# Kernel optimization log

Measured on AMD Instinct MI355X. Metric: run time of the kernel, lower is better.

Reference implementation:

```python
import jax, jax.numpy as jnp
import numpy as np

N_NODES = 50000
N_EDGES = 800000
IN_FEATS = 64
HIDDEN = 64
NUM_CLASSES = 32


def _graph_conv(x, src, dst, W, b, n_nodes):
    # DGL GraphConv, norm='both', allow_zero_in_degree=True:
    # out = D_in^{-1/2} * (A^T @ (D_out^{-1/2} * x)) @ W + b, degrees clamped to >=1
    e = src.shape[0]
    ones = jnp.ones((e,), dtype=x.dtype)
    out_deg = jax.ops.segment_sum(ones, src, num_segments=n_nodes)
    in_deg = jax.ops.segment_sum(ones, dst, num_segments=n_nodes)
    norm_src = jax.lax.rsqrt(jnp.maximum(out_deg, 1.0))[:, None]
    norm_dst = jax.lax.rsqrt(jnp.maximum(in_deg, 1.0))[:, None]
    h = x * norm_src                                   # [N, d]
    agg = jax.ops.segment_sum(h[src], dst, num_segments=n_nodes)  # gather+scatter over edges
    return (agg * norm_dst) @ W + b


def setup_inputs() -> dict:
    key = jax.random.key(0)
    k1, k2, k3, k4, k5 = jax.random.split(key, 5)
    features = jax.random.normal(k1, (N_NODES, IN_FEATS), dtype=jnp.float32)
    src = jax.random.randint(k2, (N_EDGES,), 0, N_NODES, dtype=jnp.int32)
    dst = jax.random.randint(k3, (N_EDGES,), 0, N_NODES, dtype=jnp.int32)
    W1 = jax.random.normal(k4, (IN_FEATS, HIDDEN), dtype=jnp.float32) * (1.0 / np.sqrt(IN_FEATS))
    b1 = jnp.zeros((HIDDEN,), dtype=jnp.float32)
    W2 = jax.random.normal(k5, (HIDDEN, NUM_CLASSES), dtype=jnp.float32) * (1.0 / np.sqrt(HIDDEN))
    b2 = jnp.zeros((NUM_CLASSES,), dtype=jnp.float32)
    return {"features": features, "src": src, "dst": dst,
            "W1": W1, "b1": b1, "W2": W2, "b2": b2}


def reference(features, src, dst, W1, b1, W2, b2) -> jnp.ndarray:
    n = features.shape[0]
    h = jax.nn.relu(_graph_conv(features, src, dst, W1, b1, n))
    out = _graph_conv(h, src, dst, W2, b2, n)
    # single canonical etype -> mean over one-element stack is identity
    return out
```

## Files before the change

### kernel.cpp

```cpp
#include <hip/hip_runtime.h>
#include <hip/hip_bf16.h>

#define N_NODES 50000
#define N_EDGES 800000
#define F 64
#define C 32
#define CAP 48

#define NPB   200
#define EPB   4000
#define NBUCK 196

#define G1_BLOCKS 2048

static __device__ __forceinline__ float bflo(int u) {
    return __uint_as_float(((unsigned)u) << 16);
}
static __device__ __forceinline__ float bfhi(int u) {
    return __uint_as_float(((unsigned)u) & 0xffff0000u);
}
static __device__ __forceinline__ unsigned short f2bf(float f) {
    __hip_bfloat16 h = __float2bfloat16(f);
    return *reinterpret_cast<unsigned short*>(&h);
}

__global__ void part_count_kernel(const int* __restrict__ src, const int* __restrict__ dst,
                                  int* __restrict__ bcnt_d, int* __restrict__ bcnt_s) {
    __shared__ int hd[NBUCK], hs[NBUCK];
    int t = threadIdx.x;
    for (int i = t; i < NBUCK; i += 256) { hd[i] = 0; hs[i] = 0; }
    __syncthreads();
    int b0 = blockIdx.x * EPB;
    for (int i = b0 + t; i < b0 + EPB; i += 256) {
        atomicAdd(&hd[dst[i] >> 8], 1);
        atomicAdd(&hs[src[i] >> 8], 1);
    }
    __syncthreads();
    for (int i = t; i < NBUCK; i += 256) {
        bcnt_d[i * NPB + blockIdx.x] = hd[i];
        bcnt_s[i * NPB + blockIdx.x] = hs[i];
    }
}

__global__ void part_scan_kernel(const int* __restrict__ bcnt_d, const int* __restrict__ bcnt_s,
                                 int* __restrict__ eoff_d, int* __restrict__ eoff_s,
                                 int* __restrict__ base_d, int* __restrict__ base_s) {
    __shared__ int tot_d[NBUCK], tot_s[NBUCK], bd[NBUCK + 1], bs[NBUCK + 1];
    int t = threadIdx.x;
    if (t < NBUCK) {
        int run = 0;
        for (int q = 0; q < NPB / 4; q++) {
            int4 v = *reinterpret_cast<const int4*>(bcnt_d + t * NPB + 4 * q);
            int4 o;
            o.x = run; run += v.x;
            o.y = run; run += v.y;
            o.z = run; run += v.z;
            o.w = run; run += v.w;
            *reinterpret_cast<int4*>(eoff_d + t * NPB + 4 * q) = o;
        }
        tot_d[t] = run;
        run = 0;
        for (int q = 0; q < NPB / 4; q++) {
            int4 v = *reinterpret_cast<const int4*>(bcnt_s + t * NPB + 4 * q);
            int4 o;
            o.x = run; run += v.x;
            o.y = run; run += v.y;
            o.z = run; run += v.z;
            o.w = run; run += v.w;
            *reinterpret_cast<int4*>(eoff_s + t * NPB + 4 * q) = o;
        }
        tot_s[t] = run;
    }
    __syncthreads();
    if (t == 0) {
        int r = 0;
        for (int b = 0; b < NBUCK; b++) { bd[b] = r; r += tot_d[b]; }
        bd[NBUCK] = r;
        r = 0;
        for (int b = 0; b < NBUCK; b++) { bs[b] = r; r += tot_s[b]; }
        bs[NBUCK] = r;
    }
    __syncthreads();
    if (t < NBUCK + 1) { base_d[t] = bd[t]; base_s[t] = bs[t]; }
}

__global__ void part_scatter_kernel(const int* __restrict__ src, const int* __restrict__ dst,
                                    const int* __restrict__ eoff_d, const int* __restrict__ eoff_s,
                                    const int* __restrict__ base_d, const int* __restrict__ base_s,
                                    int* __restrict__ edge_d, unsigned char* __restrict__ edge_s) {
    __shared__ int cd[NBUCK], cs[NBUCK];
    int t = threadIdx.x;
    for (int i = t; i < NBUCK; i += 256) {
        cd[i] = base_d[i] + eoff_d[i * NPB + blockIdx.x];
        cs[i] = base_s[i] + eoff_s[i * NPB + blockIdx.x];
    }
    __syncthreads();
    int b0 = blockIdx.x * EPB;
    for (int i = b0 + t; i < b0 + EPB; i += 256) {
        int d = dst[i], s = src[i];
        int p = atomicAdd(&cd[d >> 8], 1);
        edge_d[p] = ((d & 255) << 16) | s;
        int q = atomicAdd(&cs[s >> 8], 1);
        edge_s[q] = (unsigned char)(s & 255);
    }
}

__global__ void bucket_build_kernel(const int* __restrict__ edge_d,
                                    const unsigned char* __restrict__ edge_s,
                                    const int* __restrict__ base_d, const int* __restrict__ base_s,
                                    int* __restrict__ csr, int* __restrict__ cnt,
                                    float* __restrict__ norm_dst, float* __restrict__ norm_src) {
    __shared__ int cur[256];
    __shared__ int hs[256];
    int t = threadIdx.x;
    int bucket = blockIdx.x;
    cur[t] = 0;
    hs[t] = 0;
    __syncthreads();
    int lo = base_d[bucket], hi = base_d[bucket + 1];
    for (int i = lo + t; i < hi; i += 256) {
        int pd = edge_d[i];
        int dlow = pd >> 16;
        int s = pd & 0xFFFF;
        int pos = atomicAdd(&cur[dlow], 1);
        if (pos < CAP) csr[(size_t)(bucket * 256 + dlow) * CAP + pos] = s;
    }
    int slo = base_s[bucket], shi = base_s[bucket + 1];
    for (int i = slo + t; i < shi; i += 256) {
        atomicAdd(&hs[edge_s[i]], 1);
    }
    __syncthreads();
    int node = bucket * 256 + t;
    if (node < N_NODES) {
        int c = cur[t] < CAP ? cur[t] : CAP;
        cnt[node] = c;
        norm_dst[node] = rsqrtf(fmaxf((float)c, 1.0f));
        norm_src[node] = rsqrtf(fmaxf((float)hs[t], 1.0f));
    }
}

__global__ void gemm_y_kernel(const float* __restrict__ x,
                              const float* __restrict__ ns,
                              const float* __restrict__ W,
                              __hip_bfloat16* __restrict__ y) {
    __shared__ float sW[F * F];
    __shared__ float srow[16][F];
    int t = threadIdx.x;
    for (int i = t; i < F * F; i += 256) sW[i] = W[i];
    int j = t & 63;
    int w = t >> 6;
    int base = blockIdx.x * 16;
    for (int r = w; r < 16; r += 4) srow[r][j] = x[(size_t)(base + r) * F + j];
    __syncthreads();
    float a0 = 0, a1 = 0, a2 = 0, a3 = 0;
#pragma unroll
    for (int k = 0; k < F; k++) {
        float wv = sW[k * F + j];
        a0 += srow[w * 4 + 0][k] * wv;
        a1 += srow[w * 4 + 1][k] * wv;
        a2 += srow[w * 4 + 2][k] * wv;
        a3 += srow[w * 4 + 3][k] * wv;
    }
    int n0 = base + w * 4;
    y[(size_t)(n0 + 0) * F + j] = __float2bfloat16(a0 * ns[n0 + 0]);
    y[(size_t)(n0 + 1) * F + j] = __float2bfloat16(a1 * ns[n0 + 1]);
    y[(size_t)(n0 + 2) * F + j] = __float2bfloat16(a2 * ns[n0 + 2]);
    y[(size_t)(n0 + 3) * F + j] = __float2bfloat16(a3 * ns[n0 + 3]);
}

__global__ void gather64_gemv_kernel(const __hip_bfloat16* __restrict__ y,
                                     const int* __restrict__ csr,
                                     const int* __restrict__ cnt,
                                     const float* __restrict__ norm_dst,
                                     const float* __restrict__ norm_src,
                                     const float* __restrict__ b1,
                                     const float* __restrict__ W2,
                                     __hip_bfloat16* __restrict__ gt) {
    __shared__ float sW[F * C];
    int t = threadIdx.x;
    for (int i = t; i < F * C; i += 256) sW[i] = W2[i];
    __syncthreads();
    int w    = t >> 6;
    int lane = t & 63;
    int g  = lane >> 3;
    int fo = (lane & 7) * 8;
    int j    = lane & 31;
    int half = lane >> 5;
    const float4 b1a = *reinterpret_cast<const float4*>(b1 + fo);
    const float4 b1b = *reinterpret_cast<const float4*>(b1 + fo + 4);
    const unsigned short* ytab = reinterpret_cast<const unsigned short*>(y);

    for (int node = blockIdx.x * 4 + w; node < N_NODES; node += G1_BLOCKS * 4) {
        int n = cnt[node];
        const int* row = csr + (size_t)node * CAP;
        float a0 = 0.f, a1 = 0.f, a2 = 0.f, a3 = 0.f,
              a4 = 0.f, a5 = 0.f, a6 = 0.f, a7 = 0.f;

#define G1_ROUND(i)                                                          \
        {                                                                    \
            int ee = (i) * 8 + g;                                            \
            int rv = row[ee];                 \
            int ss = (ee < n) ? rv : 0;                                      \
            float m = (ee < n) ? 1.f : 0.f;                                  \
            const int4 v = *reinterpret_cast<const int4*>(                   \
                ytab + (size_t)ss * F + fo);                                 \
            a0 = fmaf(m, bflo(v.x), a0); a1 = fmaf(m, bfhi(v.x), a1);        \
            a2 = fmaf(m, bflo(v.y), a2); a3 = fmaf(m, bfhi(v.y), a3);        \
            a4 = fmaf(m, bflo(v.z), a4); a5 = fmaf(m, bfhi(v.z), a5);        \
            a6 = fmaf(m, bflo(v.w), a6); a7 = fmaf(m, bfhi(v.w), a7);        \
        }
        G1_ROUND(0)
        G1_ROUND(1)
        if (n > 16) {
            G1_ROUND(2)
            G1_ROUND(3)
            if (n > 32) {
                G1_ROUND(4)
                G1_ROUND(5)
            }
        }
#undef G1_ROUND

#define G1_RED(mk)                                                           \
        a0 += __shfl_xor(a0, mk); a1 += __shfl_xor(a1, mk);                  \
        a2 += __shfl_xor(a2, mk); a3 += __shfl_xor(a3, mk);                  \
        a4 += __shfl_xor(a4, mk); a5 += __shfl_xor(a5, mk);                  \
        a6 += __shfl_xor(a6, mk); a7 += __shfl_xor(a7, mk);
        G1_RED(8)
        G1_RED(16)
        G1_RED(32)
#undef G1_RED

        float nd = norm_dst[node], ns = norm_src[node];
        float hh[8];
        hh[0] = fmaxf(fmaf(a0, nd, b1a.x), 0.f) * ns;
        hh[1] = fmaxf(fmaf(a1, nd, b1a.y), 0.f) * ns;
        hh[2] = fmaxf(fmaf(a2, nd, b1a.z), 0.f) * ns;
        hh[3] = fmaxf(fmaf(a3, nd, b1a.w), 0.f) * ns;
        hh[4] = fmaxf(fmaf(a4, nd, b1b.x), 0.f) * ns;
        hh[5] = fmaxf(fmaf(a5, nd, b1b.y), 0.f) * ns;
        hh[6] = fmaxf(fmaf(a6, nd, b1b.z), 0.f) * ns;
        hh[7] = fmaxf(fmaf(a7, nd, b1b.w), 0.f) * ns;

        float o = 0.f;
#pragma unroll
        for (int k = 0; k < 32; k++) {
            float hv = __shfl(hh[k & 7], (half << 2) + (k >> 3));
            o = fmaf(hv, sW[(half * 32 + k) * C + j], o);
        }
        o += __shfl_down(o, 32);
        if (half == 0)
            __builtin_nontemporal_store(f2bf(o),
                reinterpret_cast<unsigned short*>(gt) + (size_t)node * C + j);
    }
}

__global__ void gather_out_kernel(const __hip_bfloat16* __restrict__ gt,
                                  const int* __restrict__ csr,
                                  const int* __restrict__ cnt,
                                  const float* __restrict__ norm_dst,
                                  const float* __restrict__ b2,
                                  float* __restrict__ out) {
    int t = threadIdx.x;
    int w = t >> 6;
    int lane = t & 63;
    int node = blockIdx.x * 4 + w;
    int g  = lane >> 3;
    int fo = (lane & 7) * 4;
    const unsigned short* tab = reinterpret_cast<const unsigned short*>(gt);
    int n = cnt[node];
    const int* row = csr + (size_t)node * CAP;
    float a0 = 0.f, a1 = 0.f, a2 = 0.f, a3 = 0.f;

#define G2_ROUND(i)                                                          \
    {                                                                        \
        int ee = (i) * 8 + g;                                                \
        int rv = row[ee];                                                    \
        int ss = (ee < n) ? rv : 0;                                          \
        float m = (ee < n) ? 1.f : 0.f;                                      \
        const int2 v = *reinterpret_cast<const int2*>(                       \
            tab + (size_t)ss * C + fo);                                      \
        a0 = fmaf(m, bflo(v.x), a0); a1 = fmaf(m, bfhi(v.x), a1);            \
        a2 = fmaf(m, bflo(v.y), a2); a3 = fmaf(m, bfhi(v.y), a3);            \
    }
    G2_ROUND(0)
    G2_ROUND(1)
    if (n > 16) {
        G2_ROUND(2)
        G2_ROUND(3)
        if (n > 32) {
            G2_ROUND(4)
            G2_ROUND(5)
        }
    }
#undef G2_ROUND

    a0 += __shfl_xor(a0, 8);  a1 += __shfl_xor(a1, 8);
    a2 += __shfl_xor(a2, 8);  a3 += __shfl_xor(a3, 8);
    a0 += __shfl_xor(a0, 16); a1 += __shfl_xor(a1, 16);
    a2 += __shfl_xor(a2, 16); a3 += __shfl_xor(a3, 16);
    a0 += __shfl_xor(a0, 32); a1 += __shfl_xor(a1, 32);
    a2 += __shfl_xor(a2, 32); a3 += __shfl_xor(a3, 32);

    if (lane < 8) {
        float nd = norm_dst[node];
        const float4 bb = *reinterpret_cast<const float4*>(b2 + fo);
        float o0 = fmaf(a0, nd, bb.x);
        float o1 = fmaf(a1, nd, bb.y);
        float o2 = fmaf(a2, nd, bb.z);
        float o3 = fmaf(a3, nd, bb.w);
        unsigned long long p0 = ((unsigned long long)__float_as_uint(o0)) |
                                ((unsigned long long)__float_as_uint(o1) << 32);
        unsigned long long p1 = ((unsigned long long)__float_as_uint(o2)) |
                                ((unsigned long long)__float_as_uint(o3) << 32);
        unsigned long long* po = reinterpret_cast<unsigned long long*>(
            out + (size_t)node * C + fo);
        __builtin_nontemporal_store(p0, po);
        __builtin_nontemporal_store(p1, po + 1);
    }
}

extern "C" void kernel_launch(void* const* d_in, const int* in_sizes, int n_in,
                              void* d_out, int out_size, void* d_ws, size_t ws_size,
                              hipStream_t stream) {
    const float* features = (const float*)d_in[0];
    const int*   src      = (const int*)d_in[1];
    const int*   dst      = (const int*)d_in[2];
    const float* W1       = (const float*)d_in[3];
    const float* b1       = (const float*)d_in[4];
    const float* W2       = (const float*)d_in[5];
    const float* b2       = (const float*)d_in[6];
    float* out = (float*)d_out;

    char* p = (char*)d_ws;
    float* norm_src = (float*)p;  p += (size_t)N_NODES * 4;
    float* norm_dst = (float*)p;  p += (size_t)N_NODES * 4;
    int*   cnt      = (int*)p;    p += (size_t)N_NODES * 4;
    int*   csr      = (int*)p;    p += (size_t)N_NODES * CAP * 4;
    __hip_bfloat16* y  = (__hip_bfloat16*)p;  p += (size_t)N_NODES * F * 2;
    __hip_bfloat16* gt = (__hip_bfloat16*)p;

    int* edge_d = (int*)y;
    unsigned char* edge_s = (unsigned char*)(edge_d + N_EDGES);
    int* q = (int*)gt;
    int* bcnt_d = q;                 q += NPB * NBUCK;
    int* bcnt_s = q;                 q += NPB * NBUCK;
    int* eoff_d = q;                 q += NPB * NBUCK;
    int* eoff_s = q;                 q += NPB * NBUCK;
    int* base_d = q;                 q += NBUCK + 1;
    int* base_s = q;

    part_count_kernel<<<NPB, 256, 0, stream>>>(src, dst, bcnt_d, bcnt_s);
    part_scan_kernel<<<1, 256, 0, stream>>>(bcnt_d, bcnt_s, eoff_d, eoff_s, base_d, base_s);
    part_scatter_kernel<<<NPB, 256, 0, stream>>>(src, dst, eoff_d, eoff_s, base_d, base_s,
                                                 edge_d, edge_s);
    bucket_build_kernel<<<NBUCK, 256, 0, stream>>>(edge_d, edge_s, base_d, base_s,
                                                   csr, cnt, norm_dst, norm_src);

    gemm_y_kernel<<<N_NODES / 16, 256, 0, stream>>>(features, norm_src, W1, y);
    gather64_gemv_kernel<<<G1_BLOCKS, 256, 0, stream>>>(y, csr, cnt, norm_dst,
                                                        norm_src, b1, W2, gt);

    gather_out_kernel<<<N_NODES / 4, 256, 0, stream>>>(gt, csr, cnt, norm_dst,
                                                       b2, out);
}
```

Baseline: 209.5 us.

## Software-pipeline CSR row loads and issue all gathers unconditionally in both gather kernels

Both gather kernels now prefetch the next node's count, norms and six CSR index slots while the current node's gathers are in flight. All six gather rounds are issued without branching, with masked-out lanes reading row 0. The output gather becomes a persistent grid-stride kernel with 2048 blocks instead of one block per four nodes. This is meant to hide index-load latency and raise memory-level parallelism, at the cost of extra loads for low-degree nodes and more registers.

After: 210.0 us. Within noise of the previous version (+0.2%).

```diff
diff --git a/kernel.cpp b/kernel.cpp
--- a/kernel.cpp
+++ b/kernel.cpp
@@ -11,7 +11,8 @@
 #define EPB   4000
 #define NBUCK 196
 
-#define G1_BLOCKS 2048
+#define G1_BLOCKS   2048
+#define GOUT_BLOCKS 2048
 
 static __device__ __forceinline__ float bflo(int u) {
     return __uint_as_float(((unsigned)u) << 16);
@@ -189,37 +190,61 @@
     const float4 b1a = *reinterpret_cast<const float4*>(b1 + fo);
     const float4 b1b = *reinterpret_cast<const float4*>(b1 + fo + 4);
     const unsigned short* ytab = reinterpret_cast<const unsigned short*>(y);
-
-    for (int node = blockIdx.x * 4 + w; node < N_NODES; node += G1_BLOCKS * 4) {
-        int n = cnt[node];
-        const int* row = csr + (size_t)node * CAP;
-        float a0 = 0.f, a1 = 0.f, a2 = 0.f, a3 = 0.f,
-              a4 = 0.f, a5 = 0.f, a6 = 0.f, a7 = 0.f;
-
-#define G1_ROUND(i)                                                          \
-        {                                                                    \
-            int ee = (i) * 8 + g;                                            \
-            int rv = row[ee];                 \
-            int ss = (ee < n) ? rv : 0;                                      \
-            float m = (ee < n) ? 1.f : 0.f;                                  \
-            const int4 v = *reinterpret_cast<const int4*>(                   \
-                ytab + (size_t)ss * F + fo);                                 \
-            a0 = fmaf(m, bflo(v.x), a0); a1 = fmaf(m, bfhi(v.x), a1);        \
-            a2 = fmaf(m, bflo(v.y), a2); a3 = fmaf(m, bfhi(v.y), a3);        \
-            a4 = fmaf(m, bflo(v.z), a4); a5 = fmaf(m, bfhi(v.z), a5);        \
-            a6 = fmaf(m, bflo(v.w), a6); a7 = fmaf(m, bfhi(v.w), a7);        \
-        }
-        G1_ROUND(0)
-        G1_ROUND(1)
-        if (n > 16) {
-            G1_ROUND(2)
-            G1_ROUND(3)
-            if (n > 32) {
-                G1_ROUND(4)
-                G1_ROUND(5)
-            }
-        }
-#undef G1_ROUND
+    const int STRIDE = G1_BLOCKS * 4;
+
+    int node = blockIdx.x * 4 + w;
+    int pn = cnt[node];
+    float pnd = norm_dst[node], pns = norm_src[node];
+    const int* prow = csr + (size_t)node * CAP;
+    int pr0 = prow[g],      pr1 = prow[8 + g],  pr2 = prow[16 + g];
+    int pr3 = prow[24 + g], pr4 = prow[32 + g], pr5 = prow[40 + g];
+
+    while (node < N_NODES) {
+        int n = pn;
+        float nd = pnd, ns = pns;
+        int r0 = pr0, r1 = pr1, r2 = pr2, r3 = pr3, r4 = pr4, r5 = pr5;
+        int nxt = node + STRIDE;
+        int pf = (nxt < N_NODES) ? nxt : node;
+
+        int ss0 = (g      < n) ? r0 : 0;  float m0 = (g      < n) ? 1.f : 0.f;
+        int ss1 = (8  + g < n) ? r1 : 0;  float m1 = (8  + g < n) ? 1.f : 0.f;
+        int ss2 = (16 + g < n) ? r2 : 0;  float m2 = (16 + g < n) ? 1.f : 0.f;
+        int ss3 = (24 + g < n) ? r3 : 0;  float m3 = (24 + g < n) ? 1.f : 0.f;
+        int ss4 = (32 + g < n) ? r4 : 0;  float m4 = (32 + g < n) ? 1.f : 0.f;
+        int ss5 = (40 + g < n) ? r5 : 0;  float m5 = (40 + g < n) ? 1.f : 0.f;
+
+        const int4 v0 = *reinterpret_cast<const int4*>(ytab + (size_t)ss0 * F + fo);
+        const int4 v1 = *reinterpret_cast<const int4*>(ytab + (size_t)ss1 * F + fo);
+        const int4 v2 = *reinterpret_cast<const int4*>(ytab + (size_t)ss2 * F + fo);
+        const int4 v3 = *reinterpret_cast<const int4*>(ytab + (size_t)ss3 * F + fo);
+
+        pn  = cnt[pf];
+        pnd = norm_dst[pf];
+        pns = norm_src[pf];
+        const int* nrow = csr + (size_t)pf * CAP;
+        pr0 = nrow[g];      pr1 = nrow[8 + g];  pr2 = nrow[16 + g];
+        pr3 = nrow[24 + g]; pr4 = nrow[32 + g]; pr5 = nrow[40 + g];
+
+        float a0, a1, a2, a3, a4, a5, a6, a7;
+        a0 = m0 * bflo(v0.x); a1 = m0 * bfhi(v0.x);
+        a2 = m0 * bflo(v0.y); a3 = m0 * bfhi(v0.y);
+        a4 = m0 * bflo(v0.z); a5 = m0 * bfhi(v0.z);
+        a6 = m0 * bflo(v0.w); a7 = m0 * bfhi(v0.w);
+
+        const int4 v4 = *reinterpret_cast<const int4*>(ytab + (size_t)ss4 * F + fo);
+        const int4 v5 = *reinterpret_cast<const int4*>(ytab + (size_t)ss5 * F + fo);
+
+#define G1_ACC(vv, mm)                                                        \
+        a0 = fmaf(mm, bflo(vv.x), a0); a1 = fmaf(mm, bfhi(vv.x), a1);         \
+        a2 = fmaf(mm, bflo(vv.y), a2); a3 = fmaf(mm, bfhi(vv.y), a3);         \
+        a4 = fmaf(mm, bflo(vv.z), a4); a5 = fmaf(mm, bfhi(vv.z), a5);         \
+        a6 = fmaf(mm, bflo(vv.w), a6); a7 = fmaf(mm, bfhi(vv.w), a7);
+        G1_ACC(v1, m1)
+        G1_ACC(v2, m2)
+        G1_ACC(v3, m3)
+        G1_ACC(v4, m4)
+        G1_ACC(v5, m5)
+#undef G1_ACC
 
 #define G1_RED(mk)                                                           \
         a0 += __shfl_xor(a0, mk); a1 += __shfl_xor(a1, mk);                  \
@@ -231,7 +256,6 @@
         G1_RED(32)
 #undef G1_RED
 
-        float nd = norm_dst[node], ns = norm_src[node];
         float hh[8];
         hh[0] = fmaxf(fmaf(a0, nd, b1a.x), 0.f) * ns;
         hh[1] = fmaxf(fmaf(a1, nd, b1a.y), 0.f) * ns;
@@ -252,6 +276,7 @@
         if (half == 0)
             __builtin_nontemporal_store(f2bf(o),
                 reinterpret_cast<unsigned short*>(gt) + (size_t)node * C + j);
+        node = nxt;
     }
 }
 
@@ -264,59 +289,83 @@
     int t = threadIdx.x;
     int w = t >> 6;
     int lane = t & 63;
-    int node = blockIdx.x * 4 + w;
     int g  = lane >> 3;
     int fo = (lane & 7) * 4;
     const unsigned short* tab = reinterpret_cast<const unsigned short*>(gt);
-    int n = cnt[node];
-    const int* row = csr + (size_t)node * CAP;
-    float a0 = 0.f, a1 = 0.f, a2 = 0.f, a3 = 0.f;
-
-#define G2_ROUND(i)                                                          \
-    {                                                                        \
-        int ee = (i) * 8 + g;                                                \
-        int rv = row[ee];                                                    \
-        int ss = (ee < n) ? rv : 0;                                          \
-        float m = (ee < n) ? 1.f : 0.f;                                      \
-        const int2 v = *reinterpret_cast<const int2*>(                       \
-            tab + (size_t)ss * C + fo);                                      \
-        a0 = fmaf(m, bflo(v.x), a0); a1 = fmaf(m, bfhi(v.x), a1);            \
-        a2 = fmaf(m, bflo(v.y), a2); a3 = fmaf(m, bfhi(v.y), a3);            \
-    }
-    G2_ROUND(0)
-    G2_ROUND(1)
-    if (n > 16) {
-        G2_ROUND(2)
-        G2_ROUND(3)
-        if (n > 32) {
-            G2_ROUND(4)
-            G2_ROUND(5)
+    const float4 bb = *reinterpret_cast<const float4*>(b2 + fo);
+    const int STRIDE = GOUT_BLOCKS * 4;
+
+    int node = blockIdx.x * 4 + w;
+    int pn = cnt[node];
+    float pnd = norm_dst[node];
+    const int* prow = csr + (size_t)node * CAP;
+    int pr0 = prow[g],      pr1 = prow[8 + g],  pr2 = prow[16 + g];
+    int pr3 = prow[24 + g], pr4 = prow[32 + g], pr5 = prow[40 + g];
+
+    while (node < N_NODES) {
+        int n = pn;
+        float nd = pnd;
+        int r0 = pr0, r1 = pr1, r2 = pr2, r3 = pr3, r4 = pr4, r5 = pr5;
+        int nxt = node + STRIDE;
+        int pf = (nxt < N_NODES) ? nxt : node;
+
+        int ss0 = (g      < n) ? r0 : 0;  float m0 = (g      < n) ? 1.f : 0.f;
+        int ss1 = (8  + g < n) ? r1 : 0;  float m1 = (8  + g < n) ? 1.f : 0.f;
+        int ss2 = (16 + g < n) ? r2 : 0;  float m2 = (16 + g < n) ? 1.f : 0.f;
+        int ss3 = (24 + g < n) ? r3 : 0;  float m3 = (24 + g < n) ? 1.f : 0.f;
+        int ss4 = (32 + g < n) ? r4 : 0;  float m4 = (32 + g < n) ? 1.f : 0.f;
+        int ss5 = (40 + g < n) ? r5 : 0;  float m5 = (40 + g < n) ? 1.f : 0.f;
+
+        const int2 v0 = *reinterpret_cast<const int2*>(tab + (size_t)ss0 * C + fo);
+        const int2 v1 = *reinterpret_cast<const int2*>(tab + (size_t)ss1 * C + fo);
+        const int2 v2 = *reinterpret_cast<const int2*>(tab + (size_t)ss2 * C + fo);
+        const int2 v3 = *reinterpret_cast<const int2*>(tab + (size_t)ss3 * C + fo);
+
+        pn  = cnt[pf];
+        pnd = norm_dst[pf];
+        const int* nrow = csr + (size_t)pf * CAP;
+        pr0 = nrow[g];      pr1 = nrow[8 + g];  pr2 = nrow[16 + g];
+        pr3 = nrow[24 + g]; pr4 = nrow[32 + g]; pr5 = nrow[40 + g];
+
+        float a0, a1, a2, a3;
+        a0 = m0 * bflo(v0.x); a1 = m0 * bfhi(v0.x);
+        a2 = m0 * bflo(v0.y); a3 = m0 * bfhi(v0.y);
+
+        const int2 v4 = *reinterpret_cast<const int2*>(tab + (size_t)ss4 * C + fo);
+        const int2 v5 = *reinterpret_cast<const int2*>(tab + (size_t)ss5 * C + fo);
+
+#define G2_ACC(vv, mm)                                                        \
+        a0 = fmaf(mm, bflo(vv.x), a0); a1 = fmaf(mm, bfhi(vv.x), a1);         \
+        a2 = fmaf(mm, bflo(vv.y), a2); a3 = fmaf(mm, bfhi(vv.y), a3);
+        G2_ACC(v1, m1)
+        G2_ACC(v2, m2)
+        G2_ACC(v3, m3)
+        G2_ACC(v4, m4)
+        G2_ACC(v5, m5)
+#undef G2_ACC
+
+        a0 += __shfl_xor(a0, 8);  a1 += __shfl_xor(a1, 8);
+        a2 += __shfl_xor(a2, 8);  a3 += __shfl_xor(a3, 8);
+        a0 += __shfl_xor(a0, 16); a1 += __shfl_xor(a1, 16);
+        a2 += __shfl_xor(a2, 16); a3 += __shfl_xor(a3, 16);
+        a0 += __shfl_xor(a0, 32); a1 += __shfl_xor(a1, 32);
+        a2 += __shfl_xor(a2, 32); a3 += __shfl_xor(a3, 32);
+
+        if (lane < 8) {
+            float o0 = fmaf(a0, nd, bb.x);
+            float o1 = fmaf(a1, nd, bb.y);
+            float o2 = fmaf(a2, nd, bb.z);
+            float o3 = fmaf(a3, nd, bb.w);
+            unsigned long long p0 = ((unsigned long long)__float_as_uint(o0)) |
+                                    ((unsigned long long)__float_as_uint(o1) << 32);
+            unsigned long long p1 = ((unsigned long long)__float_as_uint(o2)) |
+                                    ((unsigned long long)__float_as_uint(o3) << 32);
+            unsigned long long* po = reinterpret_cast<unsigned long long*>(
+                out + (size_t)node * C + fo);
+            __builtin_nontemporal_store(p0, po);
+            __builtin_nontemporal_store(p1, po + 1);
         }
-    }
-#undef G2_ROUND
-
-    a0 += __shfl_xor(a0, 8);  a1 += __shfl_xor(a1, 8);
-    a2 += __shfl_xor(a2, 8);  a3 += __shfl_xor(a3, 8);
-    a0 += __shfl_xor(a0, 16); a1 += __shfl_xor(a1, 16);
-    a2 += __shfl_xor(a2, 16); a3 += __shfl_xor(a3, 16);
-    a0 += __shfl_xor(a0, 32); a1 += __shfl_xor(a1, 32);
-    a2 += __shfl_xor(a2, 32); a3 += __shfl_xor(a3, 32);
-
-    if (lane < 8) {
-        float nd = norm_dst[node];
-        const float4 bb = *reinterpret_cast<const float4*>(b2 + fo);
-        float o0 = fmaf(a0, nd, bb.x);
-        float o1 = fmaf(a1, nd, bb.y);
-        float o2 = fmaf(a2, nd, bb.z);
-        float o3 = fmaf(a3, nd, bb.w);
-        unsigned long long p0 = ((unsigned long long)__float_as_uint(o0)) |
-                                ((unsigned long long)__float_as_uint(o1) << 32);
-        unsigned long long p1 = ((unsigned long long)__float_as_uint(o2)) |
-                                ((unsigned long long)__float_as_uint(o3) << 32);
-        unsigned long long* po = reinterpret_cast<unsigned long long*>(
-            out + (size_t)node * C + fo);
-        __builtin_nontemporal_store(p0, po);
-        __builtin_nontemporal_store(p1, po + 1);
+        node = nxt;
     }
 }
 
@@ -361,6 +410,6 @@
     gather64_gemv_kernel<<<G1_BLOCKS, 256, 0, stream>>>(y, csr, cnt, norm_dst,
                                                         norm_src, b1, W2, gt);
 
-    gather_out_kernel<<<N_NODES / 4, 256, 0, stream>>>(gt, csr, cnt, norm_dst,
+    gather_out_kernel<<<GOUT_BLOCKS, 256, 0, stream>>>(gt, csr, cnt, norm_dst,
                                                        b2, out);
 }
```
